# Performance work log

Measured on AMD Instinct MI355X. Metric: run time of the kernel, lower is better.

The kernel has to match this reference:

```python
import jax, jax.numpy as jnp
import numpy as np

N = 50000          # num nodes
E = 800000         # num edges
IN_C, HID_C, OUT_C = 128, 256, 256
LN_EPS = 1e-5


def gcn_conv(x, W, b, row, col):
    """PyG GCNConv: h = D^{-1/2}(A+I)D^{-1/2} (x W) + b, self-loops added."""
    h = x @ W                                             # [N, C_out]
    deg = jax.ops.segment_sum(jnp.ones((row.shape[0],), h.dtype), col,
                              num_segments=N) + 1.0        # +1 for self-loop
    dinv = jax.lax.rsqrt(deg)                              # [N]
    msg = h[row] * (dinv[row] * dinv[col])[:, None]        # [E, C_out] gathered msgs
    agg = jax.ops.segment_sum(msg, col, num_segments=N)
    agg = agg + h * (dinv * dinv)[:, None]                 # self-loop contribution
    return agg + b


def layer_norm(x, gamma, beta):
    mu = jnp.mean(x, axis=-1, keepdims=True)
    var = jnp.mean(jnp.square(x - mu), axis=-1, keepdims=True)
    return (x - mu) * jax.lax.rsqrt(var + LN_EPS) * gamma + beta


def setup_inputs() -> dict:
    key = jax.random.key(0)
    ks = jax.random.split(key, 8)
    x = jax.random.normal(ks[0], (N, IN_C), jnp.float32)
    edge_index = jax.random.randint(ks[1], (2, E), 0, N, dtype=jnp.int64)
    W1 = jax.random.normal(ks[2], (IN_C, HID_C), jnp.float32) * (1.0 / np.sqrt(IN_C))
    b1 = jnp.zeros((HID_C,), jnp.float32)
    W2 = jax.random.normal(ks[3], (HID_C, OUT_C), jnp.float32) * (1.0 / np.sqrt(HID_C))
    b2 = jnp.zeros((OUT_C,), jnp.float32)
    ln1_g = jnp.ones((HID_C,), jnp.float32); ln1_b = jnp.zeros((HID_C,), jnp.float32)
    ln2_g = jnp.ones((OUT_C,), jnp.float32); ln2_b = jnp.zeros((OUT_C,), jnp.float32)
    proj_W = jax.random.normal(ks[4], (IN_C, OUT_C), jnp.float32) * (1.0 / np.sqrt(IN_C))
    proj_b = jnp.zeros((OUT_C,), jnp.float32)
    return {"x": x, "edge_index": edge_index, "W1": W1, "b1": b1, "W2": W2,
            "b2": b2, "ln1_g": ln1_g, "ln1_b": ln1_b, "ln2_g": ln2_g,
            "ln2_b": ln2_b, "proj_W": proj_W, "proj_b": proj_b}


def reference(x, edge_index, W1, b1, W2, b2, ln1_g, ln1_b, ln2_g, ln2_b,
              proj_W, proj_b):
    row, col = edge_index[0], edge_index[1]   # messages flow row -> col
    identity = x @ proj_W + proj_b            # self.proj (Linear, in != out)
    h = gcn_conv(x, W1, b1, row, col)
    h = jax.nn.relu(layer_norm(h, ln1_g, ln1_b))   # dropout = identity (eval)
    g = gcn_conv(h, W2, b2, row, col)
    g = layer_norm(g, ln2_g, ln2_b)
    return jax.nn.relu(g + identity)
```

## Files before the change

### kernel.cpp

```cpp
#include <hip/hip_runtime.h>

#define NN 50000
#define NE 800000
#define LN_EPS 1e-5f

using bf16x8 = __attribute__((ext_vector_type(8))) short;
using f32x4  = __attribute__((ext_vector_type(4))) float;

__device__ __forceinline__ float b2f(unsigned short u) {
    union { unsigned int i; float f; } c;
    c.i = ((unsigned int)u) << 16;
    return c.f;
}
__device__ __forceinline__ unsigned short f2b(float f) {
    union { float f; unsigned int i; } c;
    c.f = f;
    const unsigned int i = c.i;
    return (unsigned short)((i + 0x7FFFu + ((i >> 16) & 1u)) >> 16);
}

template <int ITERS>
__device__ __forceinline__ void stage_async(const short* __restrict__ g,
                                            short* __restrict__ l) {
    const int lane = threadIdx.x & 63;
    const int wv = threadIdx.x >> 6;
#pragma unroll
    for (int i = 0; i < ITERS; ++i) {
        const int u = i * 256 + wv * 64;
        __builtin_amdgcn_global_load_lds(
            (const __attribute__((address_space(1))) void*)(g + (size_t)(u + lane) * 8),
            (__attribute__((address_space(3))) void*)(l + (size_t)u * 8),
            16, 0, 0);
    }
}

__global__ __launch_bounds__(256) void cvt_k(const float* __restrict__ X,
                                             short* __restrict__ Xb, int n4) {
    const int i = blockIdx.x * 256 + threadIdx.x;
    if (i >= n4) return;
    const float4 v = ((const float4*)X)[i];
    ushort4 o;
    o.x = f2b(v.x); o.y = f2b(v.y); o.z = f2b(v.z); o.w = f2b(v.w);
    ((ushort4*)Xb)[i] = o;
}

template <int K>
__global__ __launch_bounds__(256) void pack_w_k(const float* __restrict__ W,
                                                short* __restrict__ Wp) {
    constexpr int KB = K / 32;
    const int i = blockIdx.x * 256 + threadIdx.x;
    const int j = i & 7;
    const int l = (i >> 3) & 63;
    const int t = i >> 9;
    const int kb = t % KB;
    const int nt = t / KB;
    const int k = 32 * kb + 8 * (l >> 4) + j;
    const int n = 16 * nt + (l & 15);
    Wp[i] = (short)f2b(W[(size_t)k * 256 + n]);
}

__global__ __launch_bounds__(256) void count_k(const int* __restrict__ col,
                                               int* __restrict__ rowptr) {
    const int e = blockIdx.x * 256 + threadIdx.x;
    if (e < NE) atomicAdd(&rowptr[col[e] + 1], 1);
}

__global__ __launch_bounds__(256) void block_sum_k(const int* __restrict__ p,
                                                   int* __restrict__ psum, int n) {
    __shared__ int sh[256];
    const int t = threadIdx.x;
    const int i = blockIdx.x * 256 + t;
    sh[t] = (i < n) ? p[i] : 0;
    __syncthreads();
#pragma unroll
    for (int off = 128; off > 0; off >>= 1) {
        if (t < off) sh[t] += sh[t + off];
        __syncthreads();
    }
    if (t == 0) psum[blockIdx.x] = sh[0];
}

__global__ __launch_bounds__(256) void scan_apply_k(int* __restrict__ p,
                                                    const int* __restrict__ psum,
                                                    int n, int nblk) {
    __shared__ int sh[256];
    const int t = threadIdx.x;
    const int b = blockIdx.x;
    const int i = b * 256 + t;
    sh[t] = (t < b && t < nblk) ? psum[t] : 0;
    __syncthreads();
#pragma unroll
    for (int off = 128; off > 0; off >>= 1) {
        if (t < off) sh[t] += sh[t + off];
        __syncthreads();
    }
    const int carry = sh[0];
    __syncthreads();
    sh[t] = (i < n) ? p[i] : 0;
    __syncthreads();
#pragma unroll
    for (int off = 1; off < 256; off <<= 1) {
        const int u = (t >= off) ? sh[t - off] : 0;
        __syncthreads();
        sh[t] += u;
        __syncthreads();
    }
    if (i < n) p[i] = sh[t] + carry;
}

__global__ __launch_bounds__(256) void dinv_k(const int* __restrict__ rowptr,
                                              float* __restrict__ dinv) {
    const int i = blockIdx.x * 256 + threadIdx.x;
    if (i < NN) dinv[i] = rsqrtf((float)(rowptr[i + 1] - rowptr[i]) + 1.0f);
}

__global__ __launch_bounds__(256) void fill_k(const int* __restrict__ row,
                                              const int* __restrict__ col,
                                              const float* __restrict__ dinv,
                                              int* __restrict__ rowptr,
                                              int* __restrict__ srcs,
                                              float* __restrict__ wvals) {
    const int e = blockIdx.x * 256 + threadIdx.x;
    if (e >= NE) return;
    const int rr = row[e];
    const int pos = atomicAdd(&rowptr[col[e]], 1);
    srcs[pos] = rr;
    wvals[pos] = dinv[rr];
}

__global__ __launch_bounds__(256) void gather1_k(const short* __restrict__ X,
                                                 const int* __restrict__ endptr,
                                                 const int* __restrict__ srcs,
                                                 const float* __restrict__ wvals,
                                                 const float* __restrict__ dinv,
                                                 short* __restrict__ A1) {
    const int node = blockIdx.x * 4 + (threadIdx.x >> 6);
    const int lane = threadIdx.x & 63;
    if (node >= NN) return;
    const int start = node ? endptr[node - 1] : 0;
    const int end = endptr[node];

    float a0 = 0.f, a1 = 0.f;
    int j = start;
    for (; j + 3 < end; j += 4) {
        const int s0 = srcs[j], s1 = srcs[j + 1], s2 = srcs[j + 2], s3 = srcs[j + 3];
        const float w0 = wvals[j], w1 = wvals[j + 1];
        const float w2 = wvals[j + 2], w3 = wvals[j + 3];
        const ushort2 v0 = ((const ushort2*)(X + (size_t)s0 * 128))[lane];
        const ushort2 v1 = ((const ushort2*)(X + (size_t)s1 * 128))[lane];
        const ushort2 v2 = ((const ushort2*)(X + (size_t)s2 * 128))[lane];
        const ushort2 v3 = ((const ushort2*)(X + (size_t)s3 * 128))[lane];
        a0 += b2f(v0.x) * w0 + b2f(v1.x) * w1 + b2f(v2.x) * w2 + b2f(v3.x) * w3;
        a1 += b2f(v0.y) * w0 + b2f(v1.y) * w1 + b2f(v2.y) * w2 + b2f(v3.y) * w3;
    }
    for (; j < end; ++j) {
        const int s0 = srcs[j];
        const float w0 = wvals[j];
        const ushort2 v0 = ((const ushort2*)(X + (size_t)s0 * 128))[lane];
        a0 += b2f(v0.x) * w0;
        a1 += b2f(v0.y) * w0;
    }
    const float dc = dinv[node];
    const ushort2 h = ((const ushort2*)(X + (size_t)node * 128))[lane];
    a0 = (a0 + b2f(h.x) * dc) * dc;
    a1 = (a1 + b2f(h.y) * dc) * dc;
    ushort2 o;
    o.x = f2b(a0); o.y = f2b(a1);
    ((ushort2*)A1)[(size_t)node * 64 + lane] = o;
}

__global__ __launch_bounds__(256) void gather2_k(const short* __restrict__ H,
                                                 const int* __restrict__ endptr,
                                                 const int* __restrict__ srcs,
                                                 const float* __restrict__ wvals,
                                                 const float* __restrict__ dinv,
                                                 short* __restrict__ agg) {
    const int node = blockIdx.x * 4 + (threadIdx.x >> 6);
    const int lane = threadIdx.x & 63;
    if (node >= NN) return;
    const int start = node ? endptr[node - 1] : 0;
    const int end = endptr[node];

    float a0 = 0.f, a1 = 0.f, a2 = 0.f, a3 = 0.f;
    int j = start;
    for (; j + 3 < end; j += 4) {
        const int s0 = srcs[j], s1 = srcs[j + 1], s2 = srcs[j + 2], s3 = srcs[j + 3];
        const float w0 = wvals[j], w1 = wvals[j + 1];
        const float w2 = wvals[j + 2], w3 = wvals[j + 3];
        const ushort4 v0 = ((const ushort4*)(H + (size_t)s0 * 256))[lane];
        const ushort4 v1 = ((const ushort4*)(H + (size_t)s1 * 256))[lane];
        const ushort4 v2 = ((const ushort4*)(H + (size_t)s2 * 256))[lane];
        const ushort4 v3 = ((const ushort4*)(H + (size_t)s3 * 256))[lane];
        a0 += b2f(v0.x) * w0 + b2f(v1.x) * w1 + b2f(v2.x) * w2 + b2f(v3.x) * w3;
        a1 += b2f(v0.y) * w0 + b2f(v1.y) * w1 + b2f(v2.y) * w2 + b2f(v3.y) * w3;
        a2 += b2f(v0.z) * w0 + b2f(v1.z) * w1 + b2f(v2.z) * w2 + b2f(v3.z) * w3;
        a3 += b2f(v0.w) * w0 + b2f(v1.w) * w1 + b2f(v2.w) * w2 + b2f(v3.w) * w3;
    }
    for (; j < end; ++j) {
        const int s0 = srcs[j];
        const float w0 = wvals[j];
        const ushort4 v0 = ((const ushort4*)(H + (size_t)s0 * 256))[lane];
        a0 += b2f(v0.x) * w0;
        a1 += b2f(v0.y) * w0;
        a2 += b2f(v0.z) * w0;
        a3 += b2f(v0.w) * w0;
    }
    const float dc = dinv[node];
    const ushort4 h = ((const ushort4*)(H + (size_t)node * 256))[lane];
    ushort4 o;
    o.x = f2b((a0 + b2f(h.x) * dc) * dc);
    o.y = f2b((a1 + b2f(h.y) * dc) * dc);
    o.z = f2b((a2 + b2f(h.z) * dc) * dc);
    o.w = f2b((a3 + b2f(h.w) * dc) * dc);
    ((ushort4*)agg)[(size_t)node * 64 + lane] = o;
}

template <int K, bool PROJ, bool OUT_BF16>
__global__ __launch_bounds__(256) void gemm_ln_k(
    const short* __restrict__ X, const short* __restrict__ Wp,
    const float* __restrict__ bias, const float* __restrict__ gamma,
    const float* __restrict__ beta, const short* __restrict__ Xp,
    const short* __restrict__ Wpp, const float* __restrict__ pbias,
    void* __restrict__ Yv) {
    constexpr int KB = K / 32;
    constexpr int CHUNK = 2048 * KB;
    __shared__ short lds[2][CHUNK];
    const int lane = threadIdx.x & 63;
    const int wv = threadIdx.x >> 6;
    const int row0 = blockIdx.x * 64 + wv * 16;
    const int r = row0 + (lane & 15);
    const int rc = (r < NN) ? r : (NN - 1);
    const int kof = 8 * (lane >> 4);
    const int colbase = lane & 15;

    bf16x8 a[KB];
#pragma unroll
    for (int kb = 0; kb < KB; ++kb)
        a[kb] = *(const bf16x8*)(X + (size_t)rc * K + 32 * kb + kof);
    bf16x8 ap[4];
    if (PROJ) {
#pragma unroll
        for (int kb = 0; kb < 4; ++kb)
            ap[kb] = *(const bf16x8*)(Xp + (size_t)rc * 128 + 32 * kb + kof);
    }

    stage_async<KB>(Wp, lds[0]);

    f32x4 acc[16];
#pragma unroll
    for (int c = 0; c < 4; ++c) {
        __syncthreads();
        if (c < 3)
            stage_async<KB>(Wp + (size_t)(c + 1) * CHUNK, lds[(c + 1) & 1]);
        else if (PROJ)
            stage_async<4>(Wpp, lds[0]);
        const short* buf = lds[c & 1];
#pragma unroll
        for (int ntl = 0; ntl < 4; ++ntl) {
            f32x4 cacc = {0.f, 0.f, 0.f, 0.f};
#pragma unroll
            for (int kb = 0; kb < KB; ++kb) {
                const bf16x8 b = ((const bf16x8*)buf)[(ntl * KB + kb) * 64 + lane];
                cacc = __builtin_amdgcn_mfma_f32_16x16x32_bf16(a[kb], b, cacc, 0, 0, 0);
            }
            acc[c * 4 + ntl] = cacc;
        }
    }

    float s[4] = {0.f, 0.f, 0.f, 0.f};
    float q[4] = {0.f, 0.f, 0.f, 0.f};
#pragma unroll
    for (int nt = 0; nt < 16; ++nt) {
        const float bv = bias[nt * 16 + colbase];
#pragma unroll
        for (int rg = 0; rg < 4; ++rg) {
            const float v = acc[nt][rg] + bv;
            acc[nt][rg] = v;
            s[rg] += v;
            q[rg] += v * v;
        }
    }
#pragma unroll
    for (int off = 1; off < 16; off <<= 1) {
#pragma unroll
        for (int rg = 0; rg < 4; ++rg) {
            s[rg] += __shfl_xor(s[rg], off, 64);
            q[rg] += __shfl_xor(q[rg], off, 64);
        }
    }
    float mu[4], rsd[4];
#pragma unroll
    for (int rg = 0; rg < 4; ++rg) {
        mu[rg] = s[rg] * (1.f / 256.f);
        const float var = q[rg] * (1.f / 256.f) - mu[rg] * mu[rg];
        rsd[rg] = rsqrtf(var + LN_EPS);
    }

    const int orow0 = row0 + (lane >> 4) * 4;
    if (PROJ) {
#pragma unroll
        for (int pc = 0; pc < 4; ++pc) {
            __syncthreads();
            if (pc < 3)
                stage_async<4>(Wpp + (size_t)(pc + 1) * 8192, lds[(pc + 1) & 1]);
            const short* buf = lds[pc & 1];
#pragma unroll
            for (int ntl = 0; ntl < 4; ++ntl) {
                const int nt = pc * 4 + ntl;
                f32x4 pid = {0.f, 0.f, 0.f, 0.f};
#pragma unroll
                for (int kb = 0; kb < 4; ++kb) {
                    const bf16x8 b = ((const bf16x8*)buf)[(ntl * 4 + kb) * 64 + lane];
                    pid = __builtin_amdgcn_mfma_f32_16x16x32_bf16(ap[kb], b, pid, 0, 0, 0);
                }
                const int col = nt * 16 + colbase;
                const float g = gamma[col];
                const float be = beta[col];
                const float pbv = pbias[col];
#pragma unroll
                for (int rg = 0; rg < 4; ++rg) {
                    const int orow = orow0 + rg;
                    float v = (acc[nt][rg] - mu[rg]) * rsd[rg] * g + be;
                    v += pid[rg] + pbv;
                    v = fmaxf(v, 0.f);
                    if (orow < NN) {
                        if (OUT_BF16)
                            ((short*)Yv)[(size_t)orow * 256 + col] = (short)f2b(v);
                        else
                            ((float*)Yv)[(size_t)orow * 256 + col] = v;
                    }
                }
            }
        }
    } else {
#pragma unroll
        for (int nt = 0; nt < 16; ++nt) {
            const int col = nt * 16 + colbase;
            const float g = gamma[col];
            const float be = beta[col];
#pragma unroll
            for (int rg = 0; rg < 4; ++rg) {
                const int orow = orow0 + rg;
                float v = (acc[nt][rg] - mu[rg]) * rsd[rg] * g + be;
                v = fmaxf(v, 0.f);
                if (orow < NN) {
                    if (OUT_BF16)
                        ((short*)Yv)[(size_t)orow * 256 + col] = (short)f2b(v);
                    else
                        ((float*)Yv)[(size_t)orow * 256 + col] = v;
                }
            }
        }
    }
}

extern "C" void kernel_launch(void* const* d_in, const int* in_sizes, int n_in,
                              void* d_out, int out_size, void* d_ws, size_t ws_size,
                              hipStream_t stream) {
    const float* x    = (const float*)d_in[0];
    const int*   eidx = (const int*)d_in[1];
    const float* W1   = (const float*)d_in[2];
    const float* b1   = (const float*)d_in[3];
    const float* W2   = (const float*)d_in[4];
    const float* b2   = (const float*)d_in[5];
    const float* ln1g = (const float*)d_in[6];
    const float* ln1b = (const float*)d_in[7];
    const float* ln2g = (const float*)d_in[8];
    const float* ln2b = (const float*)d_in[9];
    const float* pW   = (const float*)d_in[10];
    const float* pb   = (const float*)d_in[11];

    const int* row = eidx;
    const int* col = eidx + NE;
    float* out = (float*)d_out;

    short* xb     = (short*)d_ws;
    short* A1     = xb + (size_t)NN * 128;
    short* Bb     = A1 + (size_t)NN * 128;
    short* Ag     = Bb + (size_t)NN * 256;
    float* dinv   = (float*)(Ag + (size_t)NN * 256);
    int*   rowptr = (int*)(dinv + NN);
    int*   psum   = rowptr + NN + 4;
    int*   srcs   = psum + 256;
    float* wvals  = (float*)(srcs + NE);
    short* Wp1    = (short*)(wvals + NE);
    short* Wp2    = Wp1 + 128 * 256;
    short* Wpp    = Wp2 + 256 * 256;

    const int nscan = NN + 1;
    const int nblk = (nscan + 255) / 256;

    cvt_k<<<(NN * 128 / 4 + 255) / 256, 256, 0, stream>>>(x, xb, NN * 128 / 4);
    pack_w_k<128><<<128, 256, 0, stream>>>(W1, Wp1);
    pack_w_k<256><<<256, 256, 0, stream>>>(W2, Wp2);
    pack_w_k<128><<<128, 256, 0, stream>>>(pW, Wpp);

    hipMemsetAsync(rowptr, 0, (NN + 4) * sizeof(int), stream);
    count_k<<<(NE + 255) / 256, 256, 0, stream>>>(col, rowptr);
    block_sum_k<<<nblk, 256, 0, stream>>>(rowptr, psum, nscan);
    scan_apply_k<<<nblk, 256, 0, stream>>>(rowptr, psum, nscan, nblk);
    dinv_k<<<(NN + 255) / 256, 256, 0, stream>>>(rowptr, dinv);
    fill_k<<<(NE + 255) / 256, 256, 0, stream>>>(row, col, dinv, rowptr, srcs, wvals);

    gather1_k<<<(NN + 3) / 4, 256, 0, stream>>>(xb, rowptr, srcs, wvals, dinv, A1);
    gemm_ln_k<128, false, true><<<(NN + 63) / 64, 256, 0, stream>>>(
        A1, Wp1, b1, ln1g, ln1b, nullptr, nullptr, nullptr, Bb);

    gather2_k<<<(NN + 3) / 4, 256, 0, stream>>>(Bb, rowptr, srcs, wvals, dinv, Ag);
    gemm_ln_k<256, true, false><<<(NN + 63) / 64, 256, 0, stream>>>(
        Ag, Wp2, b2, ln2g, ln2b, xb, Wpp, pb, out);
}
```

Baseline: 286.8 us.

## Merge prep kernels, fold dinv into scan, interleave CSR src/weight pairs

Merges the x conversion and three weight-packing kernels into one prep kernel, and computes dinv inside the scan kernel from the raw counts, dropping a separate dinv launch. It also stores each CSR edge's source index and weight together as one int2, so the gather kernels issue one 8-byte load per edge instead of two separate loads. The aim is fewer kernel launches and fewer scattered index loads in the gathers. Block-range dispatch in the prep kernel is hardcoded to the problem sizes.

```diff
diff --git a/kernel.cpp b/kernel.cpp
--- a/kernel.cpp
+++ b/kernel.cpp
@@ -34,21 +34,10 @@
     }
 }
 
-__global__ __launch_bounds__(256) void cvt_k(const float* __restrict__ X,
-                                             short* __restrict__ Xb, int n4) {
-    const int i = blockIdx.x * 256 + threadIdx.x;
-    if (i >= n4) return;
-    const float4 v = ((const float4*)X)[i];
-    ushort4 o;
-    o.x = f2b(v.x); o.y = f2b(v.y); o.z = f2b(v.z); o.w = f2b(v.w);
-    ((ushort4*)Xb)[i] = o;
-}
-
 template <int K>
-__global__ __launch_bounds__(256) void pack_w_k(const float* __restrict__ W,
-                                                short* __restrict__ Wp) {
+__device__ __forceinline__ void pack_body(const float* __restrict__ W,
+                                          short* __restrict__ Wp, int i) {
     constexpr int KB = K / 32;
-    const int i = blockIdx.x * 256 + threadIdx.x;
     const int j = i & 7;
     const int l = (i >> 3) & 63;
     const int t = i >> 9;
@@ -59,6 +48,27 @@
     Wp[i] = (short)f2b(W[(size_t)k * 256 + n]);
 }
 
+__global__ __launch_bounds__(256) void prep_k(
+    const float* __restrict__ x, const float* __restrict__ W1,
+    const float* __restrict__ W2, const float* __restrict__ pW,
+    short* __restrict__ xb, short* __restrict__ Wp1,
+    short* __restrict__ Wp2, short* __restrict__ Wpp) {
+    const int b = blockIdx.x;
+    if (b < 6250) {
+        const int i = b * 256 + threadIdx.x;
+        const float4 v = ((const float4*)x)[i];
+        ushort4 o;
+        o.x = f2b(v.x); o.y = f2b(v.y); o.z = f2b(v.z); o.w = f2b(v.w);
+        ((ushort4*)xb)[i] = o;
+    } else if (b < 6250 + 128) {
+        pack_body<128>(W1, Wp1, (b - 6250) * 256 + threadIdx.x);
+    } else if (b < 6250 + 384) {
+        pack_body<256>(W2, Wp2, (b - 6378) * 256 + threadIdx.x);
+    } else {
+        pack_body<128>(pW, Wpp, (b - 6634) * 256 + threadIdx.x);
+    }
+}
+
 __global__ __launch_bounds__(256) void count_k(const int* __restrict__ col,
                                                int* __restrict__ rowptr) {
     const int e = blockIdx.x * 256 + threadIdx.x;
@@ -82,6 +92,7 @@
 
 __global__ __launch_bounds__(256) void scan_apply_k(int* __restrict__ p,
                                                     const int* __restrict__ psum,
+                                                    float* __restrict__ dinv,
                                                     int n, int nblk) {
     __shared__ int sh[256];
     const int t = threadIdx.x;
@@ -96,7 +107,9 @@
     }
     const int carry = sh[0];
     __syncthreads();
-    sh[t] = (i < n) ? p[i] : 0;
+    const int raw = (i < n) ? p[i] : 0;
+    if (i >= 1 && i < n) dinv[i - 1] = rsqrtf((float)raw + 1.0f);
+    sh[t] = raw;
     __syncthreads();
 #pragma unroll
     for (int off = 1; off < 256; off <<= 1) {
@@ -108,30 +121,24 @@
     if (i < n) p[i] = sh[t] + carry;
 }
 
-__global__ __launch_bounds__(256) void dinv_k(const int* __restrict__ rowptr,
-                                              float* __restrict__ dinv) {
-    const int i = blockIdx.x * 256 + threadIdx.x;
-    if (i < NN) dinv[i] = rsqrtf((float)(rowptr[i + 1] - rowptr[i]) + 1.0f);
-}
-
 __global__ __launch_bounds__(256) void fill_k(const int* __restrict__ row,
                                               const int* __restrict__ col,
                                               const float* __restrict__ dinv,
                                               int* __restrict__ rowptr,
-                                              int* __restrict__ srcs,
-                                              float* __restrict__ wvals) {
+                                              int2* __restrict__ pairs) {
     const int e = blockIdx.x * 256 + threadIdx.x;
     if (e >= NE) return;
     const int rr = row[e];
     const int pos = atomicAdd(&rowptr[col[e]], 1);
-    srcs[pos] = rr;
-    wvals[pos] = dinv[rr];
+    int2 pr;
+    pr.x = rr;
+    pr.y = __float_as_int(dinv[rr]);
+    pairs[pos] = pr;
 }
 
 __global__ __launch_bounds__(256) void gather1_k(const short* __restrict__ X,
                                                  const int* __restrict__ endptr,
-                                                 const int* __restrict__ srcs,
-                                                 const float* __restrict__ wvals,
+                                                 const int2* __restrict__ pairs,
                                                  const float* __restrict__ dinv,
                                                  short* __restrict__ A1) {
     const int node = blockIdx.x * 4 + (threadIdx.x >> 6);
@@ -143,20 +150,21 @@
     float a0 = 0.f, a1 = 0.f;
     int j = start;
     for (; j + 3 < end; j += 4) {
-        const int s0 = srcs[j], s1 = srcs[j + 1], s2 = srcs[j + 2], s3 = srcs[j + 3];
-        const float w0 = wvals[j], w1 = wvals[j + 1];
-        const float w2 = wvals[j + 2], w3 = wvals[j + 3];
-        const ushort2 v0 = ((const ushort2*)(X + (size_t)s0 * 128))[lane];
-        const ushort2 v1 = ((const ushort2*)(X + (size_t)s1 * 128))[lane];
-        const ushort2 v2 = ((const ushort2*)(X + (size_t)s2 * 128))[lane];
-        const ushort2 v3 = ((const ushort2*)(X + (size_t)s3 * 128))[lane];
+        const int2 p0 = pairs[j], p1 = pairs[j + 1];
+        const int2 p2 = pairs[j + 2], p3 = pairs[j + 3];
+        const float w0 = __int_as_float(p0.y), w1 = __int_as_float(p1.y);
+        const float w2 = __int_as_float(p2.y), w3 = __int_as_float(p3.y);
+        const ushort2 v0 = ((const ushort2*)(X + (size_t)p0.x * 128))[lane];
+        const ushort2 v1 = ((const ushort2*)(X + (size_t)p1.x * 128))[lane];
+        const ushort2 v2 = ((const ushort2*)(X + (size_t)p2.x * 128))[lane];
+        const ushort2 v3 = ((const ushort2*)(X + (size_t)p3.x * 128))[lane];
         a0 += b2f(v0.x) * w0 + b2f(v1.x) * w1 + b2f(v2.x) * w2 + b2f(v3.x) * w3;
         a1 += b2f(v0.y) * w0 + b2f(v1.y) * w1 + b2f(v2.y) * w2 + b2f(v3.y) * w3;
     }
     for (; j < end; ++j) {
-        const int s0 = srcs[j];
-        const float w0 = wvals[j];
-        const ushort2 v0 = ((const ushort2*)(X + (size_t)s0 * 128))[lane];
+        const int2 p0 = pairs[j];
+        const float w0 = __int_as_float(p0.y);
+        const ushort2 v0 = ((const ushort2*)(X + (size_t)p0.x * 128))[lane];
         a0 += b2f(v0.x) * w0;
         a1 += b2f(v0.y) * w0;
     }
@@ -171,8 +179,7 @@
 
 __global__ __launch_bounds__(256) void gather2_k(const short* __restrict__ H,
                                                  const int* __restrict__ endptr,
-                                                 const int* __restrict__ srcs,
-                                                 const float* __restrict__ wvals,
+                                                 const int2* __restrict__ pairs,
                                                  const float* __restrict__ dinv,
                                                  short* __restrict__ agg) {
     const int node = blockIdx.x * 4 + (threadIdx.x >> 6);
@@ -184,22 +191,23 @@
     float a0 = 0.f, a1 = 0.f, a2 = 0.f, a3 = 0.f;
     int j = start;
     for (; j + 3 < end; j += 4) {
-        const int s0 = srcs[j], s1 = srcs[j + 1], s2 = srcs[j + 2], s3 = srcs[j + 3];
-        const float w0 = wvals[j], w1 = wvals[j + 1];
-        const float w2 = wvals[j + 2], w3 = wvals[j + 3];
-        const ushort4 v0 = ((const ushort4*)(H + (size_t)s0 * 256))[lane];
-        const ushort4 v1 = ((const ushort4*)(H + (size_t)s1 * 256))[lane];
-        const ushort4 v2 = ((const ushort4*)(H + (size_t)s2 * 256))[lane];
-        const ushort4 v3 = ((const ushort4*)(H + (size_t)s3 * 256))[lane];
+        const int2 p0 = pairs[j], p1 = pairs[j + 1];
+        const int2 p2 = pairs[j + 2], p3 = pairs[j + 3];
+        const float w0 = __int_as_float(p0.y), w1 = __int_as_float(p1.y);
+        const float w2 = __int_as_float(p2.y), w3 = __int_as_float(p3.y);
+        const ushort4 v0 = ((const ushort4*)(H + (size_t)p0.x * 256))[lane];
+        const ushort4 v1 = ((const ushort4*)(H + (size_t)p1.x * 256))[lane];
+        const ushort4 v2 = ((const ushort4*)(H + (size_t)p2.x * 256))[lane];
+        const ushort4 v3 = ((const ushort4*)(H + (size_t)p3.x * 256))[lane];
         a0 += b2f(v0.x) * w0 + b2f(v1.x) * w1 + b2f(v2.x) * w2 + b2f(v3.x) * w3;
         a1 += b2f(v0.y) * w0 + b2f(v1.y) * w1 + b2f(v2.y) * w2 + b2f(v3.y) * w3;
         a2 += b2f(v0.z) * w0 + b2f(v1.z) * w1 + b2f(v2.z) * w2 + b2f(v3.z) * w3;
         a3 += b2f(v0.w) * w0 + b2f(v1.w) * w1 + b2f(v2.w) * w2 + b2f(v3.w) * w3;
     }
     for (; j < end; ++j) {
-        const int s0 = srcs[j];
-        const float w0 = wvals[j];
-        const ushort4 v0 = ((const ushort4*)(H + (size_t)s0 * 256))[lane];
+        const int2 p0 = pairs[j];
+        const float w0 = __int_as_float(p0.y);
+        const ushort4 v0 = ((const ushort4*)(H + (size_t)p0.x * 256))[lane];
         a0 += b2f(v0.x) * w0;
         a1 += b2f(v0.y) * w0;
         a2 += b2f(v0.z) * w0;
@@ -381,32 +389,26 @@
     float* dinv   = (float*)(Ag + (size_t)NN * 256);
     int*   rowptr = (int*)(dinv + NN);
     int*   psum   = rowptr + NN + 4;
-    int*   srcs   = psum + 256;
-    float* wvals  = (float*)(srcs + NE);
-    short* Wp1    = (short*)(wvals + NE);
+    int2*  pairs  = (int2*)(psum + 256);
+    short* Wp1    = (short*)(pairs + NE);
     short* Wp2    = Wp1 + 128 * 256;
     short* Wpp    = Wp2 + 256 * 256;
 
     const int nscan = NN + 1;
     const int nblk = (nscan + 255) / 256;
 
-    cvt_k<<<(NN * 128 / 4 + 255) / 256, 256, 0, stream>>>(x, xb, NN * 128 / 4);
-    pack_w_k<128><<<128, 256, 0, stream>>>(W1, Wp1);
-    pack_w_k<256><<<256, 256, 0, stream>>>(W2, Wp2);
-    pack_w_k<128><<<128, 256, 0, stream>>>(pW, Wpp);
-
     hipMemsetAsync(rowptr, 0, (NN + 4) * sizeof(int), stream);
+    prep_k<<<6762, 256, 0, stream>>>(x, W1, W2, pW, xb, Wp1, Wp2, Wpp);
     count_k<<<(NE + 255) / 256, 256, 0, stream>>>(col, rowptr);
     block_sum_k<<<nblk, 256, 0, stream>>>(rowptr, psum, nscan);
-    scan_apply_k<<<nblk, 256, 0, stream>>>(rowptr, psum, nscan, nblk);
-    dinv_k<<<(NN + 255) / 256, 256, 0, stream>>>(rowptr, dinv);
-    fill_k<<<(NE + 255) / 256, 256, 0, stream>>>(row, col, dinv, rowptr, srcs, wvals);
-
-    gather1_k<<<(NN + 3) / 4, 256, 0, stream>>>(xb, rowptr, srcs, wvals, dinv, A1);
+    scan_apply_k<<<nblk, 256, 0, stream>>>(rowptr, psum, dinv, nscan, nblk);
+    fill_k<<<(NE + 255) / 256, 256, 0, stream>>>(row, col, dinv, rowptr, pairs);
+
+    gather1_k<<<(NN + 3) / 4, 256, 0, stream>>>(xb, rowptr, pairs, dinv, A1);
     gemm_ln_k<128, false, true><<<(NN + 63) / 64, 256, 0, stream>>>(
         A1, Wp1, b1, ln1g, ln1b, nullptr, nullptr, nullptr, Bb);
 
-    gather2_k<<<(NN + 3) / 4, 256, 0, stream>>>(Bb, rowptr, srcs, wvals, dinv, Ag);
+    gather2_k<<<(NN + 3) / 4, 256, 0, stream>>>(Bb, rowptr, pairs, dinv, Ag);
     gemm_ln_k<256, true, false><<<(NN + 63) / 64, 256, 0, stream>>>(
         Ag, Wp2, b2, ln2g, ln2b, xb, Wpp, pb, out);
 }
```

Result: faster. 278.3 us (-3.0%).
